# Optimization experiments

Hardware: AMD Instinct MI355X
Metric: run time of the kernel (lower is better)

The kernel has to match this reference:

```python
import jax, jax.numpy as jnp
import numpy as np

BETA = 0.999      # EMA momentum from __init__ default
MIN_PTS = 256     # per-class minimum point count from forward()
EPS = 1e-12       # torch F.normalize eps


def _l2norm(v):
    n = jnp.sqrt(jnp.sum(v * v, axis=1, keepdims=True))
    return v / jnp.maximum(n, EPS)


def setup_inputs() -> dict:
    key = jax.random.key(0)
    ks = jax.random.split(key, 14)
    B, N, CIN = 4, 40000, 4
    ENC_H, ENC_D, PROJ_H, PRIOR_D, NC = 256, 512, 256, 128, 13
    s = 0.02
    pos = jax.random.normal(ks[0], (B, N, 3), jnp.float32)
    x = jax.random.normal(ks[1], (B, CIN, N), jnp.float32)
    y = jax.random.randint(ks[2], (B, N), 0, NC)
    # pointwise encoder stand-in (real encoder is an opaque external PointNeXt)
    W_enc1 = jax.random.normal(ks[3], (CIN + 3, ENC_H), jnp.float32) * s
    b_enc1 = jnp.zeros((ENC_H,), jnp.float32)
    W_enc2 = jax.random.normal(ks[4], (ENC_H, ENC_D), jnp.float32) * s
    b_enc2 = jnp.zeros((ENC_D,), jnp.float32)
    # projection head: Linear(512->256) ReLU Linear(256->128) ReLU
    W1 = jax.random.normal(ks[5], (ENC_D, PROJ_H), jnp.float32) * s
    b1 = jnp.zeros((PROJ_H,), jnp.float32)
    W2 = jax.random.normal(ks[6], (PROJ_H, PRIOR_D), jnp.float32) * s
    b2 = jnp.zeros((PRIOR_D,), jnp.float32)
    prior_ema = _l2norm(jax.random.uniform(ks[7], (NC, PRIOR_D), jnp.float32))
    return {"pos": pos, "x": x, "y": y,
            "W_enc1": W_enc1, "b_enc1": b_enc1, "W_enc2": W_enc2, "b_enc2": b_enc2,
            "W1": W1, "b1": b1, "W2": W2, "b2": b2, "prior_ema": prior_ema}


def reference(pos, x, y, W_enc1, b_enc1, W_enc2, b_enc2, W1, b1, W2, b2, prior_ema):
    NC = prior_ema.shape[0]
    p0 = pos.reshape(-1, pos.shape[-1])                       # [P, 3]
    f0 = jnp.transpose(x, (0, 2, 1)).reshape(-1, x.shape[1])  # [P, C]
    labels = y.reshape(-1)                                    # [P]
    # per-class counts and the >=256 validity gate (replaces the Python class loop)
    counts = jax.ops.segment_sum(jnp.ones(labels.shape, jnp.float32), labels, num_segments=NC)
    valid = counts >= MIN_PTS                                 # [NC]
    # encoder stand-in: pointwise MLP on (features, coords)
    h = jax.nn.relu(jnp.concatenate([f0, p0], axis=1) @ W_enc1 + b_enc1)
    enc = jax.nn.relu(h @ W_enc2 + b_enc2)                    # [P, 512]
    # projection head + L2 normalize
    g = jax.nn.relu(enc @ W1 + b1)
    feat = jax.nn.relu(g @ W2 + b2)                           # [P, 128]
    feat = _l2norm(feat)
    # current_prior: features + float label column (-1 marks dropped classes)
    lbl_eff = jnp.where(valid[labels], labels, -1)
    current_prior = jnp.concatenate([feat, lbl_eff[:, None].astype(feat.dtype)], axis=1)
    # _ema: detached per-class segment mean, keep old prior for empty/invalid classes
    fsg = jax.lax.stop_gradient(feat)
    sums = jax.ops.segment_sum(fsg, labels, num_segments=NC)  # [NC, 128]
    means = sums / jnp.maximum(counts, 1.0)[:, None]
    cur = jnp.where(valid[:, None], means, prior_ema)
    new_prior = _l2norm(BETA * prior_ema + (1.0 - BETA) * cur)
    return current_prior, new_prior
```

## Files before the change

kernel.cpp:

```cpp
#include <hip/hip_runtime.h>
#include <hip/hip_bf16.h>

#define P_TOTAL 160000
#define NPB     40000
#define NCLS    13
#define TP      64
#define NBLK    (P_TOTAL / TP)

typedef __attribute__((ext_vector_type(8))) short bf16x8;
typedef __attribute__((ext_vector_type(4))) float f32x4;

__device__ __forceinline__ ushort f2bf(float f) {
  union { float f; unsigned u; } v; v.f = f;
  return (ushort)((v.u + 0x8000) >> 16);
}

__device__ __forceinline__ void transpose_tile(const float* __restrict__ src,
                                               ushort* __restrict__ dst,
                                               int K, int N, int tile, ushort (*t)[33]) {
  int ntx = N >> 5;
  int n0 = (tile % ntx) << 5, k0 = (tile / ntx) << 5;
  int KB = K >> 5;
  int c = threadIdx.x & 31, r = threadIdx.x >> 5;
  #pragma unroll
  for (int rr = 0; rr < 32; rr += 8)
    t[r + rr][c] = f2bf(src[(k0 + r + rr) * N + n0 + c]);
  __syncthreads();
  #pragma unroll
  for (int rr = 0; rr < 32; rr += 8) {
    int n = n0 + r + rr, k = k0 + c;
    dst[((n >> 4) * KB + (k >> 5)) * 512 + (n & 15) * 32 + (k & 31)] = t[c][r + rr];
  }
}

__global__ void prep_all_kernel(const float* __restrict__ We1, const float* __restrict__ We2,
                                const float* __restrict__ W1,  const float* __restrict__ W2,
                                const int* __restrict__ y,
                                ushort* __restrict__ WT1, ushort* __restrict__ WT2,
                                ushort* __restrict__ WT3, ushort* __restrict__ WT4,
                                int* __restrict__ counts) {
  __shared__ ushort t[32][33];
  __shared__ int h[NCLS];
  int b = blockIdx.x, tid = threadIdx.x;
  if (b < 128)       transpose_tile(We2, WT2, 256, 512, b, t);
  else if (b < 256)  transpose_tile(W1,  WT3, 512, 256, b - 128, t);
  else if (b < 288)  transpose_tile(W2,  WT4, 256, 128, b - 256, t);
  else if (b == 288) {
    for (int i = tid; i < 8192; i += 256) {
      int n = i >> 5, k = i & 31;
      WT1[(n >> 4) * 512 + (n & 15) * 32 + k] = (k < 7) ? f2bf(We1[k * 256 + n]) : (ushort)0;
    }
  } else {
    if (tid < NCLS) h[tid] = 0;
    __syncthreads();
    for (int i = (b - 289) * 256 + tid; i < P_TOTAL; i += 127 * 256)
      atomicAdd(&h[y[i]], 1);
    __syncthreads();
    if (tid < NCLS) atomicAdd(&counts[tid], h[tid]);
  }
}

__global__ __launch_bounds__(512, 4) void main_kernel(
    const float* __restrict__ pos, const float* __restrict__ x, const int* __restrict__ y,
    const float* __restrict__ be1, const float* __restrict__ be2,
    const float* __restrict__ b1,  const float* __restrict__ b2,
    const ushort* __restrict__ WT1, const ushort* __restrict__ WT2,
    const ushort* __restrict__ WT3, const ushort* __restrict__ WT4,
    const int* __restrict__ counts, float* __restrict__ gsums, int* __restrict__ done,
    const float* __restrict__ prior, float* __restrict__ out) {
  __shared__ ushort actbuf[TP * 264];
  __shared__ ushort chunkbuf[TP * 136];
  __shared__ float  inv_norm[TP];
  __shared__ float  lbl_eff[TP];
  __shared__ int    lbl[TP];
  __shared__ float  invn[NCLS];
  __shared__ int    is_last;

  const int tid  = threadIdx.x;
  const int wave = tid >> 6, lane = tid & 63;
  const int quad = lane >> 4, mrow = lane & 15;
  const long p0 = (long)blockIdx.x * TP;
  const int bb = (int)(p0 / NPB);
  const int n0 = (int)(p0 % NPB);
  const f32x4 zero = {0.f, 0.f, 0.f, 0.f};

  for (int i = tid; i < TP * 40; i += 512) {
    int r = i / 40, k = i - r * 40;
    float v = 0.f;
    if (k < 4)      v = x[(bb * 4 + k) * NPB + n0 + r];
    else if (k < 7) v = pos[(p0 + r) * 3 + (k - 4)];
    chunkbuf[r * 40 + k] = f2bf(v);
  }
  if (tid < TP) lbl[tid] = y[p0 + tid];
  __syncthreads();

  {
    f32x4 acc1[4][2];
    #pragma unroll
    for (int mt = 0; mt < 4; mt++) { acc1[mt][0] = zero; acc1[mt][1] = zero; }
    const int kl = quad << 3;
    bf16x8 af[4], bw[2];
    #pragma unroll
    for (int mt = 0; mt < 4; mt++)
      af[mt] = *(const bf16x8*)(&chunkbuf[0] + (mt * 16 + mrow) * 40 + kl);
    #pragma unroll
    for (int nt = 0; nt < 2; nt++)
      bw[nt] = *(const bf16x8*)(WT1 + (wave * 2 + nt) * 512 + mrow * 32 + kl);
    #pragma unroll
    for (int nt = 0; nt < 2; nt++)
      #pragma unroll
      for (int mt = 0; mt < 4; mt++)
        acc1[mt][nt] = __builtin_amdgcn_mfma_f32_16x16x32_bf16(af[mt], bw[nt], acc1[mt][nt], 0, 0, 0);
    #pragma unroll
    for (int nt = 0; nt < 2; nt++) {
      int n = wave * 32 + nt * 16 + mrow;
      float bv = be1[n];
      #pragma unroll
      for (int mt = 0; mt < 4; mt++)
        #pragma unroll
        for (int r = 0; r < 4; r++)
          actbuf[(mt * 16 + quad * 4 + r) * 264 + n] = f2bf(fmaxf(acc1[mt][nt][r] + bv, 0.f));
    }
  }
  __syncthreads();

  f32x4 acc3[4][2];
  #pragma unroll
  for (int mt = 0; mt < 4; mt++) { acc3[mt][0] = zero; acc3[mt][1] = zero; }

  ushort* const cb = &chunkbuf[0];
  for (int c = 0; c < 4; c++) {
    f32x4 acc2[4];
    #pragma unroll
    for (int mt = 0; mt < 4; mt++) acc2[mt] = zero;
    #pragma unroll
    for (int ks = 0; ks < 8; ks++) {
      const int kl = ks * 32 + (quad << 3);
      bf16x8 af[4];
      #pragma unroll
      for (int mt = 0; mt < 4; mt++)
        af[mt] = *(const bf16x8*)(actbuf + (mt * 16 + mrow) * 264 + kl);
      bf16x8 bw = *(const bf16x8*)(WT2 + ((c * 8 + wave) * 8 + ks) * 512 + mrow * 32 + (quad << 3));
      #pragma unroll
      for (int mt = 0; mt < 4; mt++)
        acc2[mt] = __builtin_amdgcn_mfma_f32_16x16x32_bf16(af[mt], bw, acc2[mt], 0, 0, 0);
    }
    if (c) __syncthreads();
    {
      int lc = wave * 16 + mrow;
      float bv = be2[c * 128 + lc];
      #pragma unroll
      for (int mt = 0; mt < 4; mt++)
        #pragma unroll
        for (int r = 0; r < 4; r++)
          cb[(mt * 16 + quad * 4 + r) * 136 + lc] = f2bf(fmaxf(acc2[mt][r] + bv, 0.f));
    }
    __syncthreads();
    #pragma unroll
    for (int ks = 0; ks < 4; ks++) {
      const int kl = ks * 32 + (quad << 3);
      bf16x8 af[4], bw[2];
      #pragma unroll
      for (int mt = 0; mt < 4; mt++)
        af[mt] = *(const bf16x8*)(cb + (mt * 16 + mrow) * 136 + kl);
      #pragma unroll
      for (int nt = 0; nt < 2; nt++)
        bw[nt] = *(const bf16x8*)(WT3 + ((wave * 2 + nt) * 16 + c * 4 + ks) * 512 + mrow * 32 + (quad << 3));
      #pragma unroll
      for (int nt = 0; nt < 2; nt++)
        #pragma unroll
        for (int mt = 0; mt < 4; mt++)
          acc3[mt][nt] = __builtin_amdgcn_mfma_f32_16x16x32_bf16(af[mt], bw[nt], acc3[mt][nt], 0, 0, 0);
    }
  }

  #pragma unroll
  for (int nt = 0; nt < 2; nt++) {
    int n = wave * 32 + nt * 16 + mrow;
    float bv = b1[n];
    #pragma unroll
    for (int mt = 0; mt < 4; mt++)
      #pragma unroll
      for (int r = 0; r < 4; r++)
        actbuf[(mt * 16 + quad * 4 + r) * 264 + n] = f2bf(fmaxf(acc3[mt][nt][r] + bv, 0.f));
  }
  __syncthreads();

  float* const part = (float*)&chunkbuf[0];

  f32x4 acc4[4];
  #pragma unroll
  for (int mt = 0; mt < 4; mt++) acc4[mt] = zero;
  #pragma unroll
  for (int ks = 0; ks < 8; ks++) {
    const int kl = ks * 32 + (quad << 3);
    bf16x8 af[4];
    #pragma unroll
    for (int mt = 0; mt < 4; mt++)
      af[mt] = *(const bf16x8*)(actbuf + (mt * 16 + mrow) * 264 + kl);
    bf16x8 bw = *(const bf16x8*)(WT4 + (wave * 8 + ks) * 512 + mrow * 32 + (quad << 3));
    #pragma unroll
    for (int mt = 0; mt < 4; mt++)
      acc4[mt] = __builtin_amdgcn_mfma_f32_16x16x32_bf16(af[mt], bw, acc4[mt], 0, 0, 0);
  }
  const int col = wave * 16 + mrow;
  float val[4][4];
  {
    float bv = b2[col];
    #pragma unroll
    for (int mt = 0; mt < 4; mt++)
      #pragma unroll
      for (int r = 0; r < 4; r++)
        val[mt][r] = fmaxf(acc4[mt][r] + bv, 0.f);
  }

  #pragma unroll
  for (int mt = 0; mt < 4; mt++)
    #pragma unroll
    for (int r = 0; r < 4; r++) {
      float s = val[mt][r] * val[mt][r];
      s += __shfl_xor(s, 1);  s += __shfl_xor(s, 2);
      s += __shfl_xor(s, 4);  s += __shfl_xor(s, 8);
      if (mrow == 0) part[wave * TP + mt * 16 + quad * 4 + r] = s;
    }
  __syncthreads();
  if (tid < TP) {
    float ss = 0.f;
    #pragma unroll
    for (int w = 0; w < 8; w++) ss += part[w * TP + tid];
    inv_norm[tid] = 1.f / fmaxf(sqrtf(ss), 1e-12f);
    int l = lbl[tid];
    lbl_eff[tid] = (counts[l] >= 256) ? (float)l : -1.f;
  }
  __syncthreads();

  float a[NCLS];
  #pragma unroll
  for (int cc = 0; cc < NCLS; cc++) a[cc] = 0.f;
  #pragma unroll
  for (int mt = 0; mt < 4; mt++)
    #pragma unroll
    for (int r = 0; r < 4; r++) {
      int R = mt * 16 + quad * 4 + r;
      float vn = val[mt][r] * inv_norm[R];
      out[(p0 + R) * 129 + col] = vn;
      int cls = lbl[R];
      #pragma unroll
      for (int cc = 0; cc < NCLS; cc++) a[cc] += (cls == cc) ? vn : 0.f;
    }
  if (tid < TP) out[(p0 + tid) * 129 + 128] = lbl_eff[tid];
  #pragma unroll
  for (int cc = 0; cc < NCLS; cc++) {
    a[cc] += __shfl_xor(a[cc], 16);
    a[cc] += __shfl_xor(a[cc], 32);
  }
  if (quad == 0)
    #pragma unroll
    for (int cc = 0; cc < NCLS; cc++) atomicAdd(&gsums[cc * 128 + col], a[cc]);

  __syncthreads();
  if (tid == 0) {
    int old = atomicAdd(done, 1);
    is_last = (old == NBLK - 1);
  }
  __syncthreads();
  if (!is_last) return;

  float* vbuf = (float*)actbuf;
  for (int i = tid; i < NCLS * 128; i += 512) {
    float g = atomicAdd(&gsums[i], 0.f);
    int cls = i >> 7;
    int cnt = counts[cls];
    float mean = g / fmaxf((float)cnt, 1.f);
    float pr = prior[i];
    float cur = (cnt >= 256) ? mean : pr;
    vbuf[i] = 0.999f * pr + 0.001f * cur;
  }
  __syncthreads();
  if (tid < NCLS) {
    float s = 0.f;
    for (int c = 0; c < 128; c++) { float t = vbuf[tid * 128 + c]; s += t * t; }
    invn[tid] = 1.f / fmaxf(sqrtf(s), 1e-12f);
  }
  __syncthreads();
  for (int i = tid; i < NCLS * 128; i += 512)
    out[(long)P_TOTAL * 129 + i] = vbuf[i] * invn[i >> 7];
}

extern "C" void kernel_launch(void* const* d_in, const int* in_sizes, int n_in,
                              void* d_out, int out_size, void* d_ws, size_t ws_size,
                              hipStream_t stream) {
  const float* pos   = (const float*)d_in[0];
  const float* x     = (const float*)d_in[1];
  const int*   y     = (const int*)  d_in[2];
  const float* We1   = (const float*)d_in[3];
  const float* be1   = (const float*)d_in[4];
  const float* We2   = (const float*)d_in[5];
  const float* be2   = (const float*)d_in[6];
  const float* W1    = (const float*)d_in[7];
  const float* b1    = (const float*)d_in[8];
  const float* W2    = (const float*)d_in[9];
  const float* b2    = (const float*)d_in[10];
  const float* prior = (const float*)d_in[11];
  float* out = (float*)d_out;

  char* ws = (char*)d_ws;
  int*    counts = (int*)   (ws + 0);
  float*  gsums  = (float*) (ws + 256);
  int*    done   = (int*)   (ws + 7168);
  ushort* WT1    = (ushort*)(ws + 8192);
  ushort* WT2    = (ushort*)(ws + 24576);
  ushort* WT3    = (ushort*)(ws + 286720);
  ushort* WT4    = (ushort*)(ws + 548864);

  hipMemsetAsync(ws, 0, 8192, stream);
  prep_all_kernel<<<416, 256, 0, stream>>>(We1, We2, W1, W2, y, WT1, WT2, WT3, WT4, counts);
  main_kernel    <<<NBLK, 512, 0, stream>>>(pos, x, y, be1, be2, b1, b2,
                                            WT1, WT2, WT3, WT4, counts, gsums, done, prior, out);
}
```

Measured before the change: 282.8 us.

## Switch MLP chain from 16x16x32 to 32x32x16 MFMA with 2x4 wave tiling

Replaces all 16x16x32 bf16 MFMA tiles with 32x32x16 MFMA. The weight pre-transpose layout changes to 32-row by 16-k blocks, and waves are split into a 2x4 grid over rows and columns. Each wave now issues fewer, larger MFMAs and reads less LDS per FLOP for the A operand. The price is a larger per-wave output footprint, different LDS write patterns and changed epilogue reductions, which could shift register pressure and bank conflicts.

```diff
diff --git a/kernel.cpp b/kernel.cpp
--- a/kernel.cpp
+++ b/kernel.cpp
@@ -9,6 +9,7 @@
 
 typedef __attribute__((ext_vector_type(8))) short bf16x8;
 typedef __attribute__((ext_vector_type(4))) float f32x4;
+typedef __attribute__((ext_vector_type(16))) float f32x16;
 
 __device__ __forceinline__ ushort f2bf(float f) {
   union { float f; unsigned u; } v; v.f = f;
@@ -20,7 +21,7 @@
                                                int K, int N, int tile, ushort (*t)[33]) {
   int ntx = N >> 5;
   int n0 = (tile % ntx) << 5, k0 = (tile / ntx) << 5;
-  int KB = K >> 5;
+  int KB16 = K >> 4;
   int c = threadIdx.x & 31, r = threadIdx.x >> 5;
   #pragma unroll
   for (int rr = 0; rr < 32; rr += 8)
@@ -29,7 +30,7 @@
   #pragma unroll
   for (int rr = 0; rr < 32; rr += 8) {
     int n = n0 + r + rr, k = k0 + c;
-    dst[((n >> 4) * KB + (k >> 5)) * 512 + (n & 15) * 32 + (k & 31)] = t[c][r + rr];
+    dst[((n >> 5) * KB16 + (k >> 4)) * 512 + (n & 31) * 16 + (k & 15)] = t[c][r + rr];
   }
 }
 
@@ -48,7 +49,8 @@
   else if (b == 288) {
     for (int i = tid; i < 8192; i += 256) {
       int n = i >> 5, k = i & 31;
-      WT1[(n >> 4) * 512 + (n & 15) * 32 + k] = (k < 7) ? f2bf(We1[k * 256 + n]) : (ushort)0;
+      WT1[((n >> 5) * 2 + (k >> 4)) * 512 + (n & 31) * 16 + (k & 15)] =
+          (k < 7) ? f2bf(We1[k * 256 + n]) : (ushort)0;
     }
   } else {
     if (tid < NCLS) h[tid] = 0;
@@ -78,11 +80,11 @@
 
   const int tid  = threadIdx.x;
   const int wave = tid >> 6, lane = tid & 63;
-  const int quad = lane >> 4, mrow = lane & 15;
+  const int lane31 = lane & 31, hi = lane >> 5;
+  const int wh = wave >> 2, wq = wave & 3;
   const long p0 = (long)blockIdx.x * TP;
   const int bb = (int)(p0 / NPB);
   const int n0 = (int)(p0 % NPB);
-  const f32x4 zero = {0.f, 0.f, 0.f, 0.f};
 
   for (int i = tid; i < TP * 40; i += 512) {
     int r = i / 40, k = i - r * 40;
@@ -95,139 +97,113 @@
   __syncthreads();
 
   {
-    f32x4 acc1[4][2];
-    #pragma unroll
-    for (int mt = 0; mt < 4; mt++) { acc1[mt][0] = zero; acc1[mt][1] = zero; }
-    const int kl = quad << 3;
-    bf16x8 af[4], bw[2];
-    #pragma unroll
-    for (int mt = 0; mt < 4; mt++)
-      af[mt] = *(const bf16x8*)(&chunkbuf[0] + (mt * 16 + mrow) * 40 + kl);
-    #pragma unroll
-    for (int nt = 0; nt < 2; nt++)
-      bw[nt] = *(const bf16x8*)(WT1 + (wave * 2 + nt) * 512 + mrow * 32 + kl);
-    #pragma unroll
-    for (int nt = 0; nt < 2; nt++)
-      #pragma unroll
-      for (int mt = 0; mt < 4; mt++)
-        acc1[mt][nt] = __builtin_amdgcn_mfma_f32_16x16x32_bf16(af[mt], bw[nt], acc1[mt][nt], 0, 0, 0);
-    #pragma unroll
-    for (int nt = 0; nt < 2; nt++) {
-      int n = wave * 32 + nt * 16 + mrow;
-      float bv = be1[n];
-      #pragma unroll
-      for (int mt = 0; mt < 4; mt++)
-        #pragma unroll
-        for (int r = 0; r < 4; r++)
-          actbuf[(mt * 16 + quad * 4 + r) * 264 + n] = f2bf(fmaxf(acc1[mt][nt][r] + bv, 0.f));
-    }
-  }
-  __syncthreads();
-
-  f32x4 acc3[4][2];
-  #pragma unroll
-  for (int mt = 0; mt < 4; mt++) { acc3[mt][0] = zero; acc3[mt][1] = zero; }
+    f32x16 acc1[2];
+    #pragma unroll
+    for (int ct = 0; ct < 2; ct++)
+      #pragma unroll
+      for (int r = 0; r < 16; r++) acc1[ct][r] = 0.f;
+    bf16x8 af = *(const bf16x8*)(&chunkbuf[0] + (wh * 32 + lane31) * 40 + hi * 8);
+    #pragma unroll
+    for (int ct = 0; ct < 2; ct++) {
+      bf16x8 bw = *(const bf16x8*)(WT1 + ((wq * 2 + ct) * 2) * 512 + lane31 * 16 + hi * 8);
+      acc1[ct] = __builtin_amdgcn_mfma_f32_32x32x16_bf16(af, bw, acc1[ct], 0, 0, 0);
+    }
+    #pragma unroll
+    for (int ct = 0; ct < 2; ct++) {
+      int col = wq * 64 + ct * 32 + lane31;
+      float bv = be1[col];
+      #pragma unroll
+      for (int reg = 0; reg < 16; reg++) {
+        int row = wh * 32 + (reg & 3) + 8 * (reg >> 2) + 4 * hi;
+        actbuf[row * 264 + col] = f2bf(fmaxf(acc1[ct][reg] + bv, 0.f));
+      }
+    }
+  }
+  __syncthreads();
+
+  f32x16 acc3[2];
+  #pragma unroll
+  for (int ct = 0; ct < 2; ct++)
+    #pragma unroll
+    for (int r = 0; r < 16; r++) acc3[ct][r] = 0.f;
 
   ushort* const cb = &chunkbuf[0];
   for (int c = 0; c < 4; c++) {
-    f32x4 acc2[4];
-    #pragma unroll
-    for (int mt = 0; mt < 4; mt++) acc2[mt] = zero;
-    #pragma unroll
-    for (int ks = 0; ks < 8; ks++) {
-      const int kl = ks * 32 + (quad << 3);
-      bf16x8 af[4];
-      #pragma unroll
-      for (int mt = 0; mt < 4; mt++)
-        af[mt] = *(const bf16x8*)(actbuf + (mt * 16 + mrow) * 264 + kl);
-      bf16x8 bw = *(const bf16x8*)(WT2 + ((c * 8 + wave) * 8 + ks) * 512 + mrow * 32 + (quad << 3));
-      #pragma unroll
-      for (int mt = 0; mt < 4; mt++)
-        acc2[mt] = __builtin_amdgcn_mfma_f32_16x16x32_bf16(af[mt], bw, acc2[mt], 0, 0, 0);
+    f32x16 acc2;
+    #pragma unroll
+    for (int r = 0; r < 16; r++) acc2[r] = 0.f;
+    #pragma unroll
+    for (int kt = 0; kt < 16; kt++) {
+      bf16x8 af = *(const bf16x8*)(actbuf + (wh * 32 + lane31) * 264 + kt * 16 + hi * 8);
+      bf16x8 bw = *(const bf16x8*)(WT2 + ((c * 4 + wq) * 16 + kt) * 512 + lane31 * 16 + hi * 8);
+      acc2 = __builtin_amdgcn_mfma_f32_32x32x16_bf16(af, bw, acc2, 0, 0, 0);
     }
     if (c) __syncthreads();
     {
-      int lc = wave * 16 + mrow;
+      int lc = wq * 32 + lane31;
       float bv = be2[c * 128 + lc];
       #pragma unroll
-      for (int mt = 0; mt < 4; mt++)
-        #pragma unroll
-        for (int r = 0; r < 4; r++)
-          cb[(mt * 16 + quad * 4 + r) * 136 + lc] = f2bf(fmaxf(acc2[mt][r] + bv, 0.f));
+      for (int reg = 0; reg < 16; reg++) {
+        int row = wh * 32 + (reg & 3) + 8 * (reg >> 2) + 4 * hi;
+        cb[row * 136 + lc] = f2bf(fmaxf(acc2[reg] + bv, 0.f));
+      }
     }
     __syncthreads();
     #pragma unroll
-    for (int ks = 0; ks < 4; ks++) {
-      const int kl = ks * 32 + (quad << 3);
-      bf16x8 af[4], bw[2];
-      #pragma unroll
-      for (int mt = 0; mt < 4; mt++)
-        af[mt] = *(const bf16x8*)(cb + (mt * 16 + mrow) * 136 + kl);
-      #pragma unroll
-      for (int nt = 0; nt < 2; nt++)
-        bw[nt] = *(const bf16x8*)(WT3 + ((wave * 2 + nt) * 16 + c * 4 + ks) * 512 + mrow * 32 + (quad << 3));
-      #pragma unroll
-      for (int nt = 0; nt < 2; nt++)
-        #pragma unroll
-        for (int mt = 0; mt < 4; mt++)
-          acc3[mt][nt] = __builtin_amdgcn_mfma_f32_16x16x32_bf16(af[mt], bw[nt], acc3[mt][nt], 0, 0, 0);
-    }
-  }
-
-  #pragma unroll
-  for (int nt = 0; nt < 2; nt++) {
-    int n = wave * 32 + nt * 16 + mrow;
+    for (int kt = 0; kt < 8; kt++) {
+      bf16x8 af = *(const bf16x8*)(cb + (wh * 32 + lane31) * 136 + kt * 16 + hi * 8);
+      #pragma unroll
+      for (int ct = 0; ct < 2; ct++) {
+        bf16x8 bw = *(const bf16x8*)(WT3 + ((wq * 2 + ct) * 32 + c * 8 + kt) * 512 + lane31 * 16 + hi * 8);
+        acc3[ct] = __builtin_amdgcn_mfma_f32_32x32x16_bf16(af, bw, acc3[ct], 0, 0, 0);
+      }
+    }
+  }
+
+  #pragma unroll
+  for (int ct = 0; ct < 2; ct++) {
+    int n = wq * 64 + ct * 32 + lane31;
     float bv = b1[n];
     #pragma unroll
-    for (int mt = 0; mt < 4; mt++)
-      #pragma unroll
-      for (int r = 0; r < 4; r++)
-        actbuf[(mt * 16 + quad * 4 + r) * 264 + n] = f2bf(fmaxf(acc3[mt][nt][r] + bv, 0.f));
+    for (int reg = 0; reg < 16; reg++) {
+      int row = wh * 32 + (reg & 3) + 8 * (reg >> 2) + 4 * hi;
+      actbuf[row * 264 + n] = f2bf(fmaxf(acc3[ct][reg] + bv, 0.f));
+    }
   }
   __syncthreads();
 
   float* const part = (float*)&chunkbuf[0];
 
-  f32x4 acc4[4];
-  #pragma unroll
-  for (int mt = 0; mt < 4; mt++) acc4[mt] = zero;
-  #pragma unroll
-  for (int ks = 0; ks < 8; ks++) {
-    const int kl = ks * 32 + (quad << 3);
-    bf16x8 af[4];
-    #pragma unroll
-    for (int mt = 0; mt < 4; mt++)
-      af[mt] = *(const bf16x8*)(actbuf + (mt * 16 + mrow) * 264 + kl);
-    bf16x8 bw = *(const bf16x8*)(WT4 + (wave * 8 + ks) * 512 + mrow * 32 + (quad << 3));
-    #pragma unroll
-    for (int mt = 0; mt < 4; mt++)
-      acc4[mt] = __builtin_amdgcn_mfma_f32_16x16x32_bf16(af[mt], bw, acc4[mt], 0, 0, 0);
-  }
-  const int col = wave * 16 + mrow;
-  float val[4][4];
+  f32x16 acc4;
+  #pragma unroll
+  for (int r = 0; r < 16; r++) acc4[r] = 0.f;
+  #pragma unroll
+  for (int kt = 0; kt < 16; kt++) {
+    bf16x8 af = *(const bf16x8*)(actbuf + (wh * 32 + lane31) * 264 + kt * 16 + hi * 8);
+    bf16x8 bw = *(const bf16x8*)(WT4 + (wq * 16 + kt) * 512 + lane31 * 16 + hi * 8);
+    acc4 = __builtin_amdgcn_mfma_f32_32x32x16_bf16(af, bw, acc4, 0, 0, 0);
+  }
+  const int gcol = wq * 32 + lane31;
+  float val[16];
   {
-    float bv = b2[col];
-    #pragma unroll
-    for (int mt = 0; mt < 4; mt++)
-      #pragma unroll
-      for (int r = 0; r < 4; r++)
-        val[mt][r] = fmaxf(acc4[mt][r] + bv, 0.f);
-  }
-
-  #pragma unroll
-  for (int mt = 0; mt < 4; mt++)
-    #pragma unroll
-    for (int r = 0; r < 4; r++) {
-      float s = val[mt][r] * val[mt][r];
-      s += __shfl_xor(s, 1);  s += __shfl_xor(s, 2);
-      s += __shfl_xor(s, 4);  s += __shfl_xor(s, 8);
-      if (mrow == 0) part[wave * TP + mt * 16 + quad * 4 + r] = s;
-    }
+    float bv = b2[gcol];
+    #pragma unroll
+    for (int reg = 0; reg < 16; reg++) val[reg] = fmaxf(acc4[reg] + bv, 0.f);
+  }
+
+  #pragma unroll
+  for (int reg = 0; reg < 16; reg++) {
+    float s = val[reg] * val[reg];
+    s += __shfl_xor(s, 1);  s += __shfl_xor(s, 2);
+    s += __shfl_xor(s, 4);  s += __shfl_xor(s, 8);  s += __shfl_xor(s, 16);
+    if (lane31 == 0)
+      part[wq * 64 + wh * 32 + (reg & 3) + 8 * (reg >> 2) + 4 * hi] = s;
+  }
   __syncthreads();
   if (tid < TP) {
     float ss = 0.f;
     #pragma unroll
-    for (int w = 0; w < 8; w++) ss += part[w * TP + tid];
+    for (int g = 0; g < 4; g++) ss += part[g * 64 + tid];
     inv_norm[tid] = 1.f / fmaxf(sqrtf(ss), 1e-12f);
     int l = lbl[tid];
     lbl_eff[tid] = (counts[l] >= 256) ? (float)l : -1.f;
@@ -238,25 +214,20 @@
   #pragma unroll
   for (int cc = 0; cc < NCLS; cc++) a[cc] = 0.f;
   #pragma unroll
-  for (int mt = 0; mt < 4; mt++)
-    #pragma unroll
-    for (int r = 0; r < 4; r++) {
-      int R = mt * 16 + quad * 4 + r;
-      float vn = val[mt][r] * inv_norm[R];
-      out[(p0 + R) * 129 + col] = vn;
-      int cls = lbl[R];
-      #pragma unroll
-      for (int cc = 0; cc < NCLS; cc++) a[cc] += (cls == cc) ? vn : 0.f;
-    }
+  for (int reg = 0; reg < 16; reg++) {
+    int grow = wh * 32 + (reg & 3) + 8 * (reg >> 2) + 4 * hi;
+    float vn = val[reg] * inv_norm[grow];
+    out[(p0 + grow) * 129 + gcol] = vn;
+    int cls = lbl[grow];
+    #pragma unroll
+    for (int cc = 0; cc < NCLS; cc++) a[cc] += (cls == cc) ? vn : 0.f;
+  }
   if (tid < TP) out[(p0 + tid) * 129 + 128] = lbl_eff[tid];
   #pragma unroll
-  for (int cc = 0; cc < NCLS; cc++) {
-    a[cc] += __shfl_xor(a[cc], 16);
-    a[cc] += __shfl_xor(a[cc], 32);
-  }
-  if (quad == 0)
-    #pragma unroll
-    for (int cc = 0; cc < NCLS; cc++) atomicAdd(&gsums[cc * 128 + col], a[cc]);
+  for (int cc = 0; cc < NCLS; cc++) a[cc] += __shfl_xor(a[cc], 32);
+  if (hi == 0)
+    #pragma unroll
+    for (int cc = 0; cc < NCLS; cc++) atomicAdd(&gsums[cc * 128 + gcol], a[cc]);
 
   __syncthreads();
   if (tid == 0) {
```

Result: slower. 328.4 us (+16.1%).
